# Optimization experiments

Measured on AMD Instinct MI355X. Metric: run time of the kernel, lower is better.

The kernel has to match this reference:

```python
import jax, jax.numpy as jnp
from jax import lax
import numpy as np

B, C, H, W_SP = 2, 64, 80, 80
IC = C // 2  # inter_channels = 32


def _conv3x3(x, w, b):
    # x: (b,c,h,w), w: (o,c,3,3), padding=1 -> SAME
    y = lax.conv_general_dilated(x, w, (1, 1), 'SAME',
                                 dimension_numbers=('NCHW', 'OIHW', 'NCHW'))
    return y + b[None, :, None, None]


def setup_inputs() -> dict:
    key = jax.random.key(0)
    ks = jax.random.split(key, 8)
    x = jax.random.normal(ks[0], (B, C, H, W_SP), dtype=jnp.float32)
    x_t = jax.random.normal(ks[1], (B, C, H, W_SP), dtype=jnp.float32)
    # learned parameters (random, fan-in scaled; W is zero-init in the original
    # module but we use random weights so the op is numerically non-trivial)
    g_w = jax.random.normal(ks[2], (IC, C, 1, 1), dtype=jnp.float32) / np.sqrt(C)
    g_b = jax.random.normal(ks[3], (IC,), dtype=jnp.float32) * 0.01
    W_w = jax.random.normal(ks[4], (C, IC, 1, 1), dtype=jnp.float32) / np.sqrt(IC)
    W_b = jax.random.normal(ks[5], (C,), dtype=jnp.float32) * 0.01
    shared_w = jax.random.normal(ks[6], (IC, C, 3, 3), dtype=jnp.float32) / np.sqrt(9 * C)
    shared_b = jax.random.normal(ks[7], (IC,), dtype=jnp.float32) * 0.01
    return {'x': x, 'x_t': x_t, 'g_w': g_w, 'g_b': g_b,
            'W_w': W_w, 'W_b': W_b, 'shared_w': shared_w, 'shared_b': shared_b}


def reference(x, x_t, g_w, g_b, W_w, W_b, shared_w, shared_b):
    b, c, h, w = x.shape
    ic = g_w.shape[0]
    n = h * w  # flattened spatial positions
    # g: 1x1 conv on x_t -> (b, n, ic)
    g_x_t = jnp.einsum('oc,bchw->bohw', g_w[:, :, 0, 0], x_t) + g_b[None, :, None, None]
    g_x_t = g_x_t.reshape(b, ic, n).transpose(0, 2, 1)
    # shared 3x3 conv for theta (on x) and phi (on x_t)
    theta_x = _conv3x3(x, shared_w, shared_b).reshape(b, ic, n).transpose(0, 2, 1)  # (b,n,ic)
    phi_x_t = _conv3x3(x_t, shared_w, shared_b).reshape(b, ic, n)                    # (b,ic,n)
    # unscaled dot-product attention over spatial positions
    f = jnp.einsum('bnc,bcm->bnm', theta_x, phi_x_t)  # (b,n,n)
    f_div_C = jax.nn.softmax(f, axis=-1)
    y = jnp.einsum('bnm,bmc->bnc', f_div_C, g_x_t)    # (b,n,ic)
    y = y.transpose(0, 2, 1).reshape(b, ic, h, w)
    # W: 1x1 conv back to in_channels, residual add
    W_y = jnp.einsum('oc,bchw->bohw', W_w[:, :, 0, 0], y) + W_b[None, :, None, None]
    return W_y + x
```

## Files before the change

kernel.cpp:

```cpp
#include <hip/hip_runtime.h>

typedef __attribute__((ext_vector_type(8))) _Float16 half8;
typedef __attribute__((ext_vector_type(4))) _Float16 half4;
typedef __attribute__((ext_vector_type(4))) float f32x4;

#define NB 2
#define CIN 64
#define ICH 32
#define HH 80
#define WW 80
#define NSP 6400
#define KSPLIT 5
#define KRANGE 1280
#define KBLK 64
#define NITER 20
#define QBLK 32
#define QGROUPS 50

__global__ __launch_bounds__(256) void nlb_prep_kernel(
    const float* __restrict__ shared_w, const float* __restrict__ g_w,
    _Float16* __restrict__ W9f, _Float16* __restrict__ GWf)
{
    int e = blockIdx.x * 256 + threadIdx.x;
    if (e < 9 * 32 * 64) {
        int c = e & 63, o = (e >> 6) & 31, tap = e >> 11;
        W9f[e] = (_Float16)shared_w[(o * 64 + c) * 9 + tap];
    } else {
        int e2 = e - 9 * 32 * 64;
        GWf[e2] = (_Float16)g_w[e2];
    }
}

__global__ __launch_bounds__(128) void nlb_conv_mfma_kernel(
    const float* __restrict__ x, const float* __restrict__ x_t,
    const _Float16* __restrict__ W9f, const _Float16* __restrict__ GWf,
    const float* __restrict__ shared_b, const float* __restrict__ g_b,
    _Float16* __restrict__ Q, _Float16* __restrict__ K, _Float16* __restrict__ Vt)
{
    const int bid = blockIdx.x;
    const int src = bid & 1;
    const int b   = (bid >> 1) & 1;
    const int h   = bid >> 2;
    const float* __restrict__ in = src ? x_t : x;

    __shared__ _Float16 xs[3 * 82 * 64];

    const int tid = threadIdx.x;

    #pragma unroll
    for (int i = 0; i < 15; ++i) {
        int idx = tid + i * 128;
        int wc = idx % 10;
        int c  = (idx / 10) & 63;
        int rr = idx / 640;
        int hr = h + rr - 1;
        float4 v0 = make_float4(0.f, 0.f, 0.f, 0.f), v1 = v0;
        if (hr >= 0 && hr < HH) {
            const float4* p = (const float4*)(in + ((size_t)(b * CIN + c) * HH + hr) * WW + wc * 8);
            v0 = p[0]; v1 = p[1];
        }
        float vals[8] = {v0.x, v0.y, v0.z, v0.w, v1.x, v1.y, v1.z, v1.w};
        const int cb = c >> 3, cl = c & 7;
        #pragma unroll
        for (int k = 0; k < 8; ++k) {
            int wi = wc * 8 + k + 1;
            int slot = cb ^ ((wi + (wi >> 3)) & 7);
            xs[(rr * 82 + wi) * 64 + slot * 8 + cl] = (_Float16)vals[k];
        }
    }
    for (int e = tid; e < 384; e += 128) {
        int wi = (e & 1) ? 81 : 0;
        int rest = e >> 1;
        int c = rest & 63, rr = rest >> 6;
        int slot = (c >> 3) ^ ((wi + (wi >> 3)) & 7);
        xs[(rr * 82 + wi) * 64 + slot * 8 + (c & 7)] = (_Float16)0.f;
    }
    __syncthreads();

    const int wid  = tid >> 6;
    const int lane = tid & 63;
    const int g = lane >> 4, r = lane & 15;
    const int o0 = wid * 16;

    half8 aw[9][2];
    #pragma unroll
    for (int tap = 0; tap < 9; ++tap)
        #pragma unroll
        for (int ch = 0; ch < 2; ++ch)
            aw[tap][ch] = *(const half8*)(W9f + ((tap * 32 + o0 + r) * 64 + ch * 32 + g * 8));
    half8 gaf[2];
    if (src) {
        #pragma unroll
        for (int ch = 0; ch < 2; ++ch)
            gaf[ch] = *(const half8*)(GWf + ((o0 + r) * 64 + ch * 32 + g * 8));
    }

    f32x4 biasv, gbv = {0.f, 0.f, 0.f, 0.f};
    #pragma unroll
    for (int j = 0; j < 4; ++j) biasv[j] = shared_b[o0 + g * 4 + j];
    if (src) {
        #pragma unroll
        for (int j = 0; j < 4; ++j) gbv[j] = g_b[o0 + g * 4 + j];
    }

    for (int ti = 0; ti < 5; ++ti) {
        const int n0 = ti * 16;
        const int wi0 = n0 + r;
        f32x4 accE = biasv;
        f32x4 accO = {0.f, 0.f, 0.f, 0.f};
        f32x4 vacc = gbv;
        #pragma unroll
        for (int tap = 0; tap < 9; ++tap) {
            const int kh = tap / 3, kw = tap % 3;
            const int wi = wi0 + kw;
            const int swz = (wi + (wi >> 3)) & 7;
            #pragma unroll
            for (int ch = 0; ch < 2; ++ch) {
                half8 bf = *(const half8*)(&xs[(kh * 82 + wi) * 64 + (((ch * 4 + g) ^ swz) * 8)]);
                if (tap & 1) accO = __builtin_amdgcn_mfma_f32_16x16x32_f16(aw[tap][ch], bf, accO, 0, 0, 0);
                else         accE = __builtin_amdgcn_mfma_f32_16x16x32_f16(aw[tap][ch], bf, accE, 0, 0, 0);
                if (src && tap == 4)
                    vacc = __builtin_amdgcn_mfma_f32_16x16x32_f16(gaf[ch], bf, vacc, 0, 0, 0);
            }
        }
        const int n = h * WW + n0 + r;
        f32x4 acc;
        #pragma unroll
        for (int j = 0; j < 4; ++j) acc[j] = accE[j] + accO[j];
        half4 pk;
        #pragma unroll
        for (int j = 0; j < 4; ++j) pk[j] = (_Float16)acc[j];
        if (!src) {
            *(half4*)(Q + (size_t)(b * NSP + n) * ICH + o0 + g * 4) = pk;
        } else {
            *(half4*)(K + (size_t)(b * NSP + n) * ICH + o0 + g * 4) = pk;
            #pragma unroll
            for (int j = 0; j < 4; ++j)
                Vt[(size_t)(b * ICH + o0 + g * 4 + j) * NSP + n] = (_Float16)vacc[j];
        }
    }
}

#define KPAD 40
#define VPAD 72

__global__ __launch_bounds__(256) void nlb_attn_kernel(
    const _Float16* __restrict__ Q, const _Float16* __restrict__ Km,
    const _Float16* __restrict__ Vt,
    float* __restrict__ YU, float* __restrict__ ML)
{
    const int bid = blockIdx.x;
    const int tg  = bid % QGROUPS;
    const int rem = bid / QGROUPS;
    const int b = rem & 1;
    const int s = rem >> 1;

    const int tid  = threadIdx.x;
    const int wid  = tid >> 6;
    const int lane = tid & 63;
    const int g = lane >> 4, r = lane & 15;

    __shared__ __align__(16) _Float16 Kls[2][KBLK][KPAD];
    __shared__ __align__(16) _Float16 Vls[2][ICH][VPAD];

    const _Float16* __restrict__ Qb = Q  + (size_t)b * NSP * ICH;
    const _Float16* __restrict__ Kb = Km + (size_t)b * NSP * ICH + (size_t)s * KRANGE * ICH;
    const _Float16* __restrict__ Vb = Vt + (size_t)b * ICH * NSP + s * KRANGE;

    const f32x4 zero4 = {0.f, 0.f, 0.f, 0.f};

    const int q0 = tg * 128 + wid * QBLK;
    half8 qa[2];
    #pragma unroll
    for (int qf = 0; qf < 2; ++qf)
        qa[qf] = *(const half8*)(Qb + (size_t)(q0 + qf * 16 + r) * ICH + g * 8);

    f32x4 yacc[2][2];
    float m2[2], lp[2];
    #pragma unroll
    for (int qf = 0; qf < 2; ++qf) {
        yacc[qf][0] = zero4; yacc[qf][1] = zero4;
        m2[qf] = -1e30f; lp[qf] = 0.f;
    }

    const int krow = tid >> 2, kcb = tid & 3;
    const int vrow = tid >> 3, vcb = tid & 7;

    {
        half8 k0 = *(const half8*)(Kb + (size_t)krow * ICH + kcb * 8);
        half8 v0 = *(const half8*)(Vb + (size_t)vrow * NSP + vcb * 8);
        *(half8*)(&Kls[0][krow][kcb * 8]) = k0;
        *(half8*)(&Vls[0][vrow][vcb * 8]) = v0;
    }
    __syncthreads();

    int cur = 0;
    for (int it = 0; it < NITER; ++it) {
        const bool more = (it + 1 < NITER);
        half8 kst, vst;
        if (more) {
            kst = *(const half8*)(Kb + (size_t)(it + 1) * KBLK * ICH + (size_t)krow * ICH + kcb * 8);
            vst = *(const half8*)(Vb + (size_t)((it + 1) * KBLK) + (size_t)vrow * NSP + vcb * 8);
        }

        half8 kf[4];
        #pragma unroll
        for (int kh = 0; kh < 4; ++kh)
            kf[kh] = *(const half8*)(&Kls[cur][kh * 16 + r][g * 8]);
        half4 vf[4][2];
        #pragma unroll
        for (int kh = 0; kh < 4; ++kh)
            #pragma unroll
            for (int ch = 0; ch < 2; ++ch)
                vf[kh][ch] = *(const half4*)(&Vls[cur][ch * 16 + r][kh * 16 + g * 4]);

        #pragma unroll
        for (int qf = 0; qf < 2; ++qf) {
            f32x4 sa[4];
            #pragma unroll
            for (int kh = 0; kh < 4; ++kh)
                sa[kh] = __builtin_amdgcn_mfma_f32_16x16x32_f16(kf[kh], qa[qf], zero4, 0, 0, 0);
            float vmax = fmaxf(fmaxf(fmaxf(sa[0][0], sa[0][1]), fmaxf(sa[0][2], sa[0][3])),
                               fmaxf(fmaxf(sa[1][0], sa[1][1]), fmaxf(sa[1][2], sa[1][3])));
            vmax = fmaxf(vmax, fmaxf(fmaxf(fmaxf(sa[2][0], sa[2][1]), fmaxf(sa[2][2], sa[2][3])),
                                     fmaxf(fmaxf(sa[3][0], sa[3][1]), fmaxf(sa[3][2], sa[3][3]))));
            if (__any(vmax - m2[qf] > 8.f)) {
                float tm = vmax;
                tm = fmaxf(tm, __shfl_xor(tm, 16));
                tm = fmaxf(tm, __shfl_xor(tm, 32));
                float mn = fmaxf(m2[qf], tm);
                float sc = __expf(m2[qf] - mn);
                m2[qf] = mn; lp[qf] *= sc;
                #pragma unroll
                for (int j = 0; j < 4; ++j) { yacc[qf][0][j] *= sc; yacc[qf][1][j] *= sc; }
            }
            half4 pk[4];
            #pragma unroll
            for (int kh = 0; kh < 4; ++kh) {
                float ls = 0.f;
                #pragma unroll
                for (int j = 0; j < 4; ++j) {
                    float p = __expf(sa[kh][j] - m2[qf]);
                    ls += p; pk[kh][j] = (_Float16)p;
                }
                lp[qf] += ls;
            }
            #pragma unroll
            for (int kh = 0; kh < 4; ++kh)
                #pragma unroll
                for (int ch = 0; ch < 2; ++ch)
                    yacc[qf][ch] = __builtin_amdgcn_mfma_f32_16x16x16f16(
                        vf[kh][ch], pk[kh], yacc[qf][ch], 0, 0, 0);
        }

        if (more) {
            *(half8*)(&Kls[cur ^ 1][krow][kcb * 8]) = kst;
            *(half8*)(&Vls[cur ^ 1][vrow][vcb * 8]) = vst;
        }
        __syncthreads();
        cur ^= 1;
    }

    #pragma unroll
    for (int qf = 0; qf < 2; ++qf) {
        float lv = lp[qf];
        lv += __shfl_xor(lv, 16);
        lv += __shfl_xor(lv, 32);
        if (g == 0) {
            size_t base = ((size_t)(s * NB + b) * NSP + q0 + qf * 16 + r) * 2;
            ML[base + 0] = m2[qf];
            ML[base + 1] = lv;
        }
        #pragma unroll
        for (int ch = 0; ch < 2; ++ch)
            *(f32x4*)(YU + ((size_t)(s * NB + b) * NSP + q0 + qf * 16 + r) * ICH
                      + ch * 16 + g * 4) = yacc[qf][ch];
    }
}

__global__ __launch_bounds__(256) void nlb_combine_kernel(
    const float* __restrict__ YU, const float* __restrict__ ML,
    const float* __restrict__ W_w, const float* __restrict__ W_b,
    const float* __restrict__ x, float* __restrict__ out)
{
    const int bid = blockIdx.x;
    const int b = bid / 100;
    const int rowbase = (bid % 100) * 64;

    __shared__ float ylds[64][33];
    __shared__ float wwl[CIN * ICH];

    const int tid = threadIdx.x;
    for (int e = tid; e < CIN * ICH; e += 256) wwl[e] = W_w[e];

    #pragma unroll
    for (int i = 0; i < 8; ++i) {
        int idx = tid + i * 256;
        int row = idx >> 5, c = idx & 31;
        int grow = rowbase + row;
        float m[KSPLIT], lv[KSPLIT], M = -1e30f;
        #pragma unroll
        for (int s2 = 0; s2 < KSPLIT; ++s2) {
            size_t base = ((size_t)(s2 * NB + b) * NSP + grow) * 2;
            m[s2]  = ML[base + 0];
            lv[s2] = ML[base + 1];
            M = fmaxf(M, m[s2]);
        }
        float denom = 0.f, acc = 0.f;
        #pragma unroll
        for (int s2 = 0; s2 < KSPLIT; ++s2) {
            float e2 = __expf(m[s2] - M);
            denom += lv[s2] * e2;
            acc += YU[((size_t)(s2 * NB + b) * NSP + grow) * ICH + c] * e2;
        }
        ylds[row][c] = acc / denom;
    }
    __syncthreads();

    const int row = tid & 63;
    const int o0  = tid >> 6;
    #pragma unroll
    for (int k = 0; k < 16; ++k) {
        int o = o0 * 16 + k;
        size_t gi = (size_t)(b * CIN + o) * NSP + rowbase + row;
        float accv = W_b[o] + x[gi];
        #pragma unroll
        for (int c = 0; c < ICH; ++c) accv += wwl[o * ICH + c] * ylds[row][c];
        out[gi] = accv;
    }
}

extern "C" void kernel_launch(void* const* d_in, const int* in_sizes, int n_in,
                              void* d_out, int out_size, void* d_ws, size_t ws_size,
                              hipStream_t stream) {
    const float* x        = (const float*)d_in[0];
    const float* x_t      = (const float*)d_in[1];
    const float* g_w      = (const float*)d_in[2];
    const float* g_b      = (const float*)d_in[3];
    const float* W_w      = (const float*)d_in[4];
    const float* W_b      = (const float*)d_in[5];
    const float* shared_w = (const float*)d_in[6];
    const float* shared_b = (const float*)d_in[7];
    float* out = (float*)d_out;

    char* ws = (char*)d_ws;
    _Float16* Q   = (_Float16*)(ws);
    _Float16* K   = (_Float16*)(ws + 819200);
    _Float16* Vt  = (_Float16*)(ws + 1638400);
    float*    YU  = (float*)(ws + 2457600);
    float*    ML  = (float*)(ws + 10649600);
    _Float16* W9f = (_Float16*)(ws + 11161600);
    _Float16* GWf = (_Float16*)(ws + 11198464);

    hipLaunchKernelGGL(nlb_prep_kernel, dim3(80), dim3(256), 0, stream,
                       shared_w, g_w, W9f, GWf);
    hipLaunchKernelGGL(nlb_conv_mfma_kernel, dim3(320), dim3(128), 0, stream,
                       x, x_t, W9f, GWf, shared_b, g_b, Q, K, Vt);
    hipLaunchKernelGGL(nlb_attn_kernel, dim3(NB * QGROUPS * KSPLIT), dim3(256), 0, stream,
                       Q, K, Vt, YU, ML);
    hipLaunchKernelGGL(nlb_combine_kernel, dim3(200), dim3(256), 0, stream,
                       YU, ML, W_w, W_b, x, out);
}
```

Measured before the change: 67.03 us.

## Double attention key block size, widen conv to four waves, add MFMA priority

The attention kernel now processes 128 keys per iteration instead of 64, which halves the number of barriers and staging rounds. Each thread loads two K and V chunks, and V fragments are read from LDS inside the per-key-chunk loop, which keeps register pressure lower. QK MFMAs are wrapped in s_setprio to raise wave priority. The conv kernel moves to 256 threads, with waves splitting the width tiles 3/2, so the staging load is spread over more threads. The costs are more LDS per block, which may reduce occupancy, and an uneven split of work across conv waves.

```diff
diff --git a/kernel.cpp b/kernel.cpp
--- a/kernel.cpp
+++ b/kernel.cpp
@@ -12,8 +12,8 @@
 #define NSP 6400
 #define KSPLIT 5
 #define KRANGE 1280
-#define KBLK 64
-#define NITER 20
+#define KBLK 128
+#define NITER 10
 #define QBLK 32
 #define QGROUPS 50
 
@@ -31,7 +31,7 @@
     }
 }
 
-__global__ __launch_bounds__(128) void nlb_conv_mfma_kernel(
+__global__ __launch_bounds__(256) void nlb_conv_mfma_kernel(
     const float* __restrict__ x, const float* __restrict__ x_t,
     const _Float16* __restrict__ W9f, const _Float16* __restrict__ GWf,
     const float* __restrict__ shared_b, const float* __restrict__ g_b,
@@ -48,27 +48,29 @@
     const int tid = threadIdx.x;
 
     #pragma unroll
-    for (int i = 0; i < 15; ++i) {
-        int idx = tid + i * 128;
-        int wc = idx % 10;
-        int c  = (idx / 10) & 63;
-        int rr = idx / 640;
-        int hr = h + rr - 1;
-        float4 v0 = make_float4(0.f, 0.f, 0.f, 0.f), v1 = v0;
-        if (hr >= 0 && hr < HH) {
-            const float4* p = (const float4*)(in + ((size_t)(b * CIN + c) * HH + hr) * WW + wc * 8);
-            v0 = p[0]; v1 = p[1];
-        }
-        float vals[8] = {v0.x, v0.y, v0.z, v0.w, v1.x, v1.y, v1.z, v1.w};
-        const int cb = c >> 3, cl = c & 7;
-        #pragma unroll
-        for (int k = 0; k < 8; ++k) {
-            int wi = wc * 8 + k + 1;
-            int slot = cb ^ ((wi + (wi >> 3)) & 7);
-            xs[(rr * 82 + wi) * 64 + slot * 8 + cl] = (_Float16)vals[k];
-        }
-    }
-    for (int e = tid; e < 384; e += 128) {
+    for (int i = 0; i < 8; ++i) {
+        int idx = tid + i * 256;
+        if (idx < 1920) {
+            int wc = idx % 10;
+            int c  = (idx / 10) & 63;
+            int rr = idx / 640;
+            int hr = h + rr - 1;
+            float4 v0 = make_float4(0.f, 0.f, 0.f, 0.f), v1 = v0;
+            if (hr >= 0 && hr < HH) {
+                const float4* p = (const float4*)(in + ((size_t)(b * CIN + c) * HH + hr) * WW + wc * 8);
+                v0 = p[0]; v1 = p[1];
+            }
+            float vals[8] = {v0.x, v0.y, v0.z, v0.w, v1.x, v1.y, v1.z, v1.w};
+            const int cb = c >> 3, cl = c & 7;
+            #pragma unroll
+            for (int k = 0; k < 8; ++k) {
+                int wi = wc * 8 + k + 1;
+                int slot = cb ^ ((wi + (wi >> 3)) & 7);
+                xs[(rr * 82 + wi) * 64 + slot * 8 + cl] = (_Float16)vals[k];
+            }
+        }
+    }
+    for (int e = tid; e < 384; e += 256) {
         int wi = (e & 1) ? 81 : 0;
         int rest = e >> 1;
         int c = rest & 63, rr = rest >> 6;
@@ -80,7 +82,9 @@
     const int wid  = tid >> 6;
     const int lane = tid & 63;
     const int g = lane >> 4, r = lane & 15;
-    const int o0 = wid * 16;
+    const int o0 = (wid & 1) * 16;
+    const int ti_lo = (wid >> 1) ? 3 : 0;
+    const int ti_hi = (wid >> 1) ? 5 : 3;
 
     half8 aw[9][2];
     #pragma unroll
@@ -103,7 +107,7 @@
         for (int j = 0; j < 4; ++j) gbv[j] = g_b[o0 + g * 4 + j];
     }
 
-    for (int ti = 0; ti < 5; ++ti) {
+    for (int ti = ti_lo; ti < ti_hi; ++ti) {
         const int n0 = ti * 16;
         const int wi0 = n0 + r;
         f32x4 accE = biasv;
@@ -142,7 +146,7 @@
 }
 
 #define KPAD 40
-#define VPAD 72
+#define VPAD 136
 
 __global__ __launch_bounds__(256) void nlb_attn_kernel(
     const _Float16* __restrict__ Q, const _Float16* __restrict__ Km,
@@ -183,47 +187,54 @@
         m2[qf] = -1e30f; lp[qf] = 0.f;
     }
 
-    const int krow = tid >> 2, kcb = tid & 3;
-    const int vrow = tid >> 3, vcb = tid & 7;
+    const int kr0 = tid >> 1,          kc0 = (tid & 1);
+    (void)kr0; (void)kc0;
+
+    const int ka_r = tid >> 2,          ka_c = tid & 3;
+    const int kb_r = (tid + 256) >> 2,  kb_c = (tid + 256) & 3;
+    const int va_r = tid >> 4,          va_c = tid & 15;
+    const int vb_r = (tid + 256) >> 4,  vb_c = (tid + 256) & 15;
 
     {
-        half8 k0 = *(const half8*)(Kb + (size_t)krow * ICH + kcb * 8);
-        half8 v0 = *(const half8*)(Vb + (size_t)vrow * NSP + vcb * 8);
-        *(half8*)(&Kls[0][krow][kcb * 8]) = k0;
-        *(half8*)(&Vls[0][vrow][vcb * 8]) = v0;
+        *(half8*)(&Kls[0][ka_r][ka_c * 8]) = *(const half8*)(Kb + (size_t)ka_r * ICH + ka_c * 8);
+        *(half8*)(&Kls[0][kb_r][kb_c * 8]) = *(const half8*)(Kb + (size_t)kb_r * ICH + kb_c * 8);
+        *(half8*)(&Vls[0][va_r][va_c * 8]) = *(const half8*)(Vb + (size_t)va_r * NSP + va_c * 8);
+        *(half8*)(&Vls[0][vb_r][vb_c * 8]) = *(const half8*)(Vb + (size_t)vb_r * NSP + vb_c * 8);
     }
     __syncthreads();
 
     int cur = 0;
     for (int it = 0; it < NITER; ++it) {
         const bool more = (it + 1 < NITER);
-        half8 kst, vst;
+        half8 kst0, kst1, vst0, vst1;
         if (more) {
-            kst = *(const half8*)(Kb + (size_t)(it + 1) * KBLK * ICH + (size_t)krow * ICH + kcb * 8);
-            vst = *(const half8*)(Vb + (size_t)((it + 1) * KBLK) + (size_t)vrow * NSP + vcb * 8);
-        }
-
-        half8 kf[4];
-        #pragma unroll
-        for (int kh = 0; kh < 4; ++kh)
+            const _Float16* Kn = Kb + (size_t)(it + 1) * KBLK * ICH;
+            const _Float16* Vn = Vb + (size_t)(it + 1) * KBLK;
+            kst0 = *(const half8*)(Kn + (size_t)ka_r * ICH + ka_c * 8);
+            kst1 = *(const half8*)(Kn + (size_t)kb_r * ICH + kb_c * 8);
+            vst0 = *(const half8*)(Vn + (size_t)va_r * NSP + va_c * 8);
+            vst1 = *(const half8*)(Vn + (size_t)vb_r * NSP + vb_c * 8);
+        }
+
+        half8 kf[8];
+        #pragma unroll
+        for (int kh = 0; kh < 8; ++kh)
             kf[kh] = *(const half8*)(&Kls[cur][kh * 16 + r][g * 8]);
-        half4 vf[4][2];
-        #pragma unroll
-        for (int kh = 0; kh < 4; ++kh)
-            #pragma unroll
-            for (int ch = 0; ch < 2; ++ch)
-                vf[kh][ch] = *(const half4*)(&Vls[cur][ch * 16 + r][kh * 16 + g * 4]);
 
         #pragma unroll
         for (int qf = 0; qf < 2; ++qf) {
-            f32x4 sa[4];
-            #pragma unroll
-            for (int kh = 0; kh < 4; ++kh)
+            f32x4 sa[8];
+            __builtin_amdgcn_s_setprio(1);
+            #pragma unroll
+            for (int kh = 0; kh < 8; ++kh)
                 sa[kh] = __builtin_amdgcn_mfma_f32_16x16x32_f16(kf[kh], qa[qf], zero4, 0, 0, 0);
-            float vmax = fmaxf(fmaxf(fmaxf(sa[0][0], sa[0][1]), fmaxf(sa[0][2], sa[0][3])),
-                               fmaxf(fmaxf(sa[1][0], sa[1][1]), fmaxf(sa[1][2], sa[1][3])));
-            vmax = fmaxf(vmax, fmaxf(fmaxf(fmaxf(sa[2][0], sa[2][1]), fmaxf(sa[2][2], sa[2][3])),
-                                     fmaxf(fmaxf(sa[3][0], sa[3][1]), fmaxf(sa[3][2], sa[3][3]))));
+            __builtin_amdgcn_s_setprio(0);
+
+            float vmax = -1e30f;
+            #pragma unroll
+            for (int kh = 0; kh < 8; ++kh)
+                vmax = fmaxf(vmax, fmaxf(fmaxf(sa[kh][0], sa[kh][1]),
+                                         fmaxf(sa[kh][2], sa[kh][3])));
             if (__any(vmax - m2[qf] > 8.f)) {
                 float tm = vmax;
                 tm = fmaxf(tm, __shfl_xor(tm, 16));
@@ -234,28 +245,28 @@
                 #pragma unroll
                 for (int j = 0; j < 4; ++j) { yacc[qf][0][j] *= sc; yacc[qf][1][j] *= sc; }
             }
-            half4 pk[4];
-            #pragma unroll
-            for (int kh = 0; kh < 4; ++kh) {
-                float ls = 0.f;
+
+            #pragma unroll
+            for (int kh = 0; kh < 8; ++kh) {
+                half4 pk; float ls = 0.f;
                 #pragma unroll
                 for (int j = 0; j < 4; ++j) {
                     float p = __expf(sa[kh][j] - m2[qf]);
-                    ls += p; pk[kh][j] = (_Float16)p;
+                    ls += p; pk[j] = (_Float16)p;
                 }
                 lp[qf] += ls;
-            }
-            #pragma unroll
-            for (int kh = 0; kh < 4; ++kh)
-                #pragma unroll
-                for (int ch = 0; ch < 2; ++ch)
-                    yacc[qf][ch] = __builtin_amdgcn_mfma_f32_16x16x16f16(
-                        vf[kh][ch], pk[kh], yacc[qf][ch], 0, 0, 0);
+                half4 vfa = *(const half4*)(&Vls[cur][r][kh * 16 + g * 4]);
+                half4 vfb = *(const half4*)(&Vls[cur][16 + r][kh * 16 + g * 4]);
+                yacc[qf][0] = __builtin_amdgcn_mfma_f32_16x16x16f16(vfa, pk, yacc[qf][0], 0, 0, 0);
+                yacc[qf][1] = __builtin_amdgcn_mfma_f32_16x16x16f16(vfb, pk, yacc[qf][1], 0, 0, 0);
+            }
         }
 
         if (more) {
-            *(half8*)(&Kls[cur ^ 1][krow][kcb * 8]) = kst;
-            *(half8*)(&Vls[cur ^ 1][vrow][vcb * 8]) = vst;
+            *(half8*)(&Kls[cur ^ 1][ka_r][ka_c * 8]) = kst0;
+            *(half8*)(&Kls[cur ^ 1][kb_r][kb_c * 8]) = kst1;
+            *(half8*)(&Vls[cur ^ 1][va_r][va_c * 8]) = vst0;
+            *(half8*)(&Vls[cur ^ 1][vb_r][vb_c * 8]) = vst1;
         }
         __syncthreads();
         cur ^= 1;
@@ -354,7 +365,7 @@
 
     hipLaunchKernelGGL(nlb_prep_kernel, dim3(80), dim3(256), 0, stream,
                        shared_w, g_w, W9f, GWf);
-    hipLaunchKernelGGL(nlb_conv_mfma_kernel, dim3(320), dim3(128), 0, stream,
+    hipLaunchKernelGGL(nlb_conv_mfma_kernel, dim3(320), dim3(256), 0, stream,
                        x, x_t, W9f, GWf, shared_b, g_b, Q, K, Vt);
     hipLaunchKernelGGL(nlb_attn_kernel, dim3(NB * QGROUPS * KSPLIT), dim3(256), 0, stream,
                        Q, K, Vt, YU, ML);
```

Result: faster. 64.47 us (-3.8%).
